# Optimization experiments

Hardware: AMD Instinct MI355X
Metric: run time of the kernel (lower is better)

The kernel has to match this reference:

```python
import jax, jax.numpy as jnp
import numpy as np

GROUPS = 8
EPS = 1e-3  # keras GroupNormalization default epsilon


def group_norm(x, gamma, beta):
    # x: [B,H,W,C], groups over channel axis
    B, H, W, C = x.shape
    g = GROUPS
    xr = x.reshape(B, H, W, g, C // g)
    mean = jnp.mean(xr, axis=(1, 2, 4), keepdims=True)
    var = jnp.var(xr, axis=(1, 2, 4), keepdims=True)
    xn = (xr - mean) * jax.lax.rsqrt(var + EPS)
    xn = xn.reshape(B, H, W, C)
    return xn * gamma + beta


def setup_inputs() -> dict:
    key = jax.random.key(0)
    ks = jax.random.split(key, 6)
    B, H, W, C = 8, 64, 64, 64
    std = 0.02
    return {
        "x": jax.random.normal(ks[0], (B, H, W, C), dtype=jnp.float32),
        "gamma": jnp.ones((C,), dtype=jnp.float32),
        "beta": jnp.zeros((C,), dtype=jnp.float32),
        "wq": jax.random.normal(ks[1], (C, C), dtype=jnp.float32) * std,
        "bq": jnp.zeros((C,), dtype=jnp.float32),
        "wk": jax.random.normal(ks[2], (C, C), dtype=jnp.float32) * std,
        "bk": jnp.zeros((C,), dtype=jnp.float32),
        "wv": jax.random.normal(ks[3], (C, C), dtype=jnp.float32) * std,
        "bv": jnp.zeros((C,), dtype=jnp.float32),
        "wp": jax.random.normal(ks[4], (C, C), dtype=jnp.float32) * std,
        "bp": jnp.zeros((C,), dtype=jnp.float32),
    }


def reference(x, gamma, beta, wq, bq, wk, bk, wv, bv, wp, bp):
    B, H, W, C = x.shape
    scale = jnp.asarray(C, x.dtype) ** -0.5
    h = group_norm(x, gamma, beta)  # note: residual uses normalized input (as in source)
    q = h @ wq + bq
    k = h @ wk + bk
    v = h @ wv + bv
    # full O((HW)^2) score tensor, exactly as the original
    attn = jnp.einsum('bhwc,bHWc->bhwHW', q, k) * scale
    attn = jax.nn.softmax(attn.reshape(B, H, W, H * W), axis=-1)
    attn = attn.reshape(B, H, W, H, W)
    proj = jnp.einsum('bhwHW,bHWc->bhwc', attn, v)
    proj = proj @ wp + bp
    return h + proj
```

## Files before the change

kernel.cpp:

```cpp
#include <hip/hip_runtime.h>

#define NTOK 4096
#define CH 64
#define LOG2E 1.4426950408889634f
#define QK_SCALE 0.42466090014400953f

typedef __bf16 bf8 __attribute__((ext_vector_type(8)));
typedef __bf16 bf4 __attribute__((ext_vector_type(4)));
typedef _Float16 h8 __attribute__((ext_vector_type(8)));
typedef _Float16 h4 __attribute__((ext_vector_type(4)));
typedef float f4 __attribute__((ext_vector_type(4)));
typedef long lx2 __attribute__((ext_vector_type(2)));

__device__ __forceinline__ f4 mfma16(bf8 a, bf8 b, f4 c) {
    return __builtin_amdgcn_mfma_f32_16x16x32_bf16(a, b, c, 0, 0, 0);
}
__device__ __forceinline__ f4 mfma8(long a, long b, f4 c) {
    return __builtin_amdgcn_mfma_f32_16x16x32_fp8_fp8(a, b, c, 0, 0, 0);
}
__device__ __forceinline__ unsigned char to_fp8(float v) {
    return (unsigned char)(__builtin_amdgcn_cvt_pk_fp8_f32(v, v, 0, false) & 0xff);
}

__global__ __launch_bounds__(256) void pre_kernel(const float* __restrict__ wq,
                                                  const float* __restrict__ wk,
                                                  const float* __restrict__ wv,
                                                  const float* __restrict__ wp,
                                                  const float* __restrict__ x,
                                                  __bf16* __restrict__ wqt,
                                                  __bf16* __restrict__ wkt,
                                                  __bf16* __restrict__ wvt,
                                                  __bf16* __restrict__ wpt,
                                                  float* __restrict__ gpart) {
    int t = threadIdx.x;
    if (blockIdx.x < 4) {
        int m = blockIdx.x;
        const float* src = (m == 0) ? wq : (m == 1) ? wk : (m == 2) ? wv : wp;
        __bf16* dst      = (m == 0) ? wqt : (m == 1) ? wkt : (m == 2) ? wvt : wpt;
        __shared__ float s[64][65];
        for (int i = 0; i < 16; ++i) {
            int e = i * 256 + t;
            s[e >> 6][e & 63] = src[e];
        }
        __syncthreads();
        int o = t >> 2, seg = t & 3;
        for (int j = 0; j < 16; ++j) {
            int in = seg * 16 + j;
            dst[o * 64 + in] = (__bf16)s[in][o];
        }
        return;
    }
    int bid = blockIdx.x - 4;
    int b = bid >> 6, slab = bid & 63;
    const float4* xb = (const float4*)(x + (size_t)(b * NTOK + slab * 64) * CH);
    float s = 0.f, ss = 0.f;
    for (int i = 0; i < 4; ++i) {
        int row = (t >> 4) + i * 16;
        float4 v = xb[row * 16 + (t & 15)];
        s  += v.x + v.y + v.z + v.w;
        ss += v.x * v.x + v.y * v.y + v.z * v.z + v.w * v.w;
    }
    __shared__ float ls[256], lss[256];
    ls[t] = s; lss[t] = ss;
    __syncthreads();
    if (t < 8) {
        float a = 0.f, aa = 0.f;
        for (int p = 0; p < 16; ++p) {
            a  += ls[p * 16 + 2 * t]  + ls[p * 16 + 2 * t + 1];
            aa += lss[p * 16 + 2 * t] + lss[p * 16 + 2 * t + 1];
        }
        gpart[((b * 64 + slab) * 8 + t) * 2 + 0] = a;
        gpart[((b * 64 + slab) * 8 + t) * 2 + 1] = aa;
    }
}

__global__ __launch_bounds__(256) void qkv_gn(const float* __restrict__ x,
                                              const float* __restrict__ gpart,
                                              const float* __restrict__ gamma,
                                              const float* __restrict__ beta,
                                              const __bf16* __restrict__ wqt,
                                              const __bf16* __restrict__ wkt,
                                              const __bf16* __restrict__ wvt,
                                              const float* __restrict__ bq,
                                              const float* __restrict__ bk,
                                              const float* __restrict__ bv,
                                              unsigned char* __restrict__ qp,
                                              unsigned char* __restrict__ kp,
                                              unsigned char* __restrict__ vp) {
    __shared__ __bf16 W[3][64][72];
    __shared__ _Float16 Vst[64][68];
    __shared__ unsigned char Qst[64][72];
    __shared__ unsigned char Kst[64][72];
    __shared__ float red[128];
    __shared__ float sstat[16];
    __shared__ float sg[64], sb2[64];
    int t = threadIdx.x;
    size_t rowbase = (size_t)blockIdx.x * 64;
    int b = (int)(rowbase >> 12), tokbase = (int)(rowbase & 4095);
    int lane = t & 63, wave = t >> 6, quad = lane >> 4, l15 = lane & 15;
    int row = wave * 16 + l15;

    const float* xr = x + (rowbase + row) * 64;
    float4 xl0 = *(const float4*)(xr + quad * 8);
    float4 xl1 = *(const float4*)(xr + quad * 8 + 4);
    float4 xh0 = *(const float4*)(xr + 32 + quad * 8);
    float4 xh1 = *(const float4*)(xr + 32 + quad * 8 + 4);

    for (int m = 0; m < 3; ++m) {
        const __bf16* src = (m == 0) ? wqt : (m == 1) ? wkt : wvt;
        for (int i = 0; i < 2; ++i) {
            int e = i * 256 + t, rr = e >> 3, ch = e & 7;
            *(bf8*)&W[m][rr][ch * 8] = *(const bf8*)(src + rr * 64 + ch * 8);
        }
    }
    if (t < 64) { sg[t] = gamma[t]; sb2[t] = beta[t]; }
    if (t < 64) {
        int gi = t & 7, c = t >> 3;
        const float2* gp = (const float2*)gpart + (size_t)b * 512 + gi;
        float a = 0.f, aa = 0.f;
        for (int p = c * 8; p < c * 8 + 8; ++p) {
            float2 v = gp[(size_t)p * 8];
            a += v.x; aa += v.y;
        }
        red[t * 2] = a; red[t * 2 + 1] = aa;
    }
    __syncthreads();
    if (t < 8) {
        float a = 0.f, aa = 0.f;
        for (int c = 0; c < 8; ++c) {
            a  += red[(c * 8 + t) * 2];
            aa += red[(c * 8 + t) * 2 + 1];
        }
        float mean = a * (1.f / 32768.f);
        float var = aa * (1.f / 32768.f) - mean * mean;
        sstat[t * 2 + 0] = mean;
        sstat[t * 2 + 1] = rsqrtf(var + 1e-3f);
    }
    __syncthreads();

    bf8 a0, a1;
    {
        float mlo = sstat[quad * 2], rlo = sstat[quad * 2 + 1];
        float mhi = sstat[(4 + quad) * 2], rhi = sstat[(4 + quad) * 2 + 1];
        float xl[8] = {xl0.x, xl0.y, xl0.z, xl0.w, xl1.x, xl1.y, xl1.z, xl1.w};
        float xh[8] = {xh0.x, xh0.y, xh0.z, xh0.w, xh1.x, xh1.y, xh1.z, xh1.w};
#pragma unroll
        for (int j = 0; j < 8; ++j) {
            int c = quad * 8 + j;
            a0[j] = (__bf16)((xl[j] - mlo) * sg[c] * rlo + sb2[c]);
            a1[j] = (__bf16)((xh[j] - mhi) * sg[32 + c] * rhi + sb2[32 + c]);
        }
    }

    for (int m = 0; m < 3; ++m) {
        const float* bias = (m == 0) ? bq : (m == 1) ? bk : bv;
        float sc = (m == 2) ? 1.0f : QK_SCALE;
        for (int tt = 0; tt < 4; ++tt) {
            int col = l15 + 16 * tt;
            bf8 b0 = *(const bf8*)&W[m][col][quad * 8];
            bf8 b1 = *(const bf8*)&W[m][col][32 + quad * 8];
            f4 acc = {0.f, 0.f, 0.f, 0.f};
            acc = mfma16(a0, b0, acc);
            acc = mfma16(a1, b1, acc);
            float bb = bias[col];
            if (m == 2) {
                for (int r = 0; r < 4; ++r)
                    Vst[col][wave * 16 + quad * 4 + r] = (_Float16)(acc[r] + bb);
            } else if (m == 1) {
                for (int r = 0; r < 4; ++r)
                    Kst[wave * 16 + quad * 4 + r][col] = to_fp8((acc[r] + bb) * sc);
            } else {
                for (int r = 0; r < 4; ++r)
                    Qst[wave * 16 + quad * 4 + r][col] = to_fp8((acc[r] + bb) * sc);
            }
        }
    }
    __syncthreads();
    {
        const unsigned char* krow = &Kst[wave * 16 + l15][0];
        lx2 kk; kk[0] = *(const long*)(krow + quad * 8);
        kk[1] = *(const long*)(krow + 32 + quad * 8);
        *(lx2*)(kp + (((size_t)b * 256 + (tokbase >> 4) + wave) * 64 + lane) * 16) = kk;
        const unsigned char* qrow = &Qst[wave * 16 + l15][0];
        lx2 qq; qq[0] = *(const long*)(qrow + quad * 8);
        qq[1] = *(const long*)(qrow + 32 + quad * 8);
        *(lx2*)(qp + (((size_t)b * 256 + (tokbase >> 4) + wave) * 64 + lane) * 16) = qq;
    }
    {
        int d = wave * 16 + l15;
        for (int kb = 0; kb < 2; ++kb) {
            h4 lo = *(const h4*)&Vst[d][kb * 32 + quad * 4];
            h4 hi = *(const h4*)&Vst[d][kb * 32 + 16 + quad * 4];
            int d0 = __builtin_amdgcn_cvt_pk_fp8_f32((float)lo[0], (float)lo[1], 0, false);
            d0     = __builtin_amdgcn_cvt_pk_fp8_f32((float)lo[2], (float)lo[3], d0, true);
            int d1 = __builtin_amdgcn_cvt_pk_fp8_f32((float)hi[0], (float)hi[1], 0, false);
            d1     = __builtin_amdgcn_cvt_pk_fp8_f32((float)hi[2], (float)hi[3], d1, true);
            long v8 = (long)(unsigned int)d0 | ((long)d1 << 32);
            int kt = (tokbase >> 5) + kb;
            *(long*)(vp + ((((size_t)b * 128 + kt) * 2 + (wave >> 1)) * 64 + lane) * 16
                        + (wave & 1) * 8) = v8;
        }
    }
}

__device__ __forceinline__ void load_kv(const unsigned char* kpw, const unsigned char* vpw,
                                        long kf[4], long vf[4]) {
    lx2 a = *(const lx2*)(kpw);
    lx2 b = *(const lx2*)(kpw + 1024);
    lx2 c = *(const lx2*)(vpw);
    lx2 d = *(const lx2*)(vpw + 1024);
    kf[0] = a[0]; kf[1] = a[1]; kf[2] = b[0]; kf[3] = b[1];
    vf[0] = c[0]; vf[1] = c[1]; vf[2] = d[0]; vf[3] = d[1];
}

__device__ __forceinline__ void compute32(const long kf[4], const long vf[4],
                                          const long aqlo[8], const long aqhi[8],
                                          long ones, f4 acc[8][4], f4 acc_li[8]) {
#pragma unroll
    for (int s = 0; s < 8; ++s) {
        f4 St0 = {0.f, 0.f, 0.f, 0.f};
        f4 St1 = {0.f, 0.f, 0.f, 0.f};
        St0 = mfma8(kf[0], aqlo[s], St0);
        St0 = mfma8(kf[1], aqhi[s], St0);
        St1 = mfma8(kf[2], aqlo[s], St1);
        St1 = mfma8(kf[3], aqhi[s], St1);
        float p00 = __builtin_amdgcn_exp2f(St0[0]);
        float p01 = __builtin_amdgcn_exp2f(St0[1]);
        float p02 = __builtin_amdgcn_exp2f(St0[2]);
        float p03 = __builtin_amdgcn_exp2f(St0[3]);
        float p10 = __builtin_amdgcn_exp2f(St1[0]);
        float p11 = __builtin_amdgcn_exp2f(St1[1]);
        float p12 = __builtin_amdgcn_exp2f(St1[2]);
        float p13 = __builtin_amdgcn_exp2f(St1[3]);
        int d0 = __builtin_amdgcn_cvt_pk_fp8_f32(p00, p01, 0, false);
        d0     = __builtin_amdgcn_cvt_pk_fp8_f32(p02, p03, d0, true);
        int d1 = __builtin_amdgcn_cvt_pk_fp8_f32(p10, p11, 0, false);
        d1     = __builtin_amdgcn_cvt_pk_fp8_f32(p12, p13, d1, true);
        long pf = (long)(unsigned int)d0 | ((long)d1 << 32);
        acc_li[s] = mfma8(ones, pf, acc_li[s]);
        acc[s][0] = mfma8(vf[0], pf, acc[s][0]);
        acc[s][1] = mfma8(vf[1], pf, acc[s][1]);
        acc[s][2] = mfma8(vf[2], pf, acc[s][2]);
        acc[s][3] = mfma8(vf[3], pf, acc[s][3]);
    }
}

__global__ __launch_bounds__(256, 1) void attn_final(const unsigned char* __restrict__ qp,
                                                     const unsigned char* __restrict__ kp,
                                                     const unsigned char* __restrict__ vp,
                                                     const __bf16* __restrict__ wpt,
                                                     const float* __restrict__ bp,
                                                     const float* __restrict__ x,
                                                     const float* __restrict__ gpart,
                                                     const float* __restrict__ gamma,
                                                     const float* __restrict__ beta,
                                                     float* __restrict__ out) {
    __shared__ _Float16 Om[2][128][72];
    __shared__ float sS[2][128];
    __shared__ __bf16 Wl[64][72];
    __shared__ __bf16 Ol[128][72];
    __shared__ float red[128];
    __shared__ float sstat[16], sg[64], sb[64];

    int bid = blockIdx.x;
    int qt = bid >> 3, b = bid & 7;
    int t = threadIdx.x, lane = t & 63, w = t >> 6, quad = lane >> 4, l15 = lane & 15;

    for (int i = 0; i < 2; ++i) {
        int e = i * 256 + t, row = e >> 3, ch = e & 7;
        *(bf8*)&Wl[row][ch * 8] = *(const bf8*)(wpt + row * 64 + ch * 8);
    }
    if (t < 64) { sg[t] = gamma[t]; sb[t] = beta[t]; }
    if (t < 64) {
        int gi = t & 7, c = t >> 3;
        const float2* gp = (const float2*)gpart + (size_t)b * 512 + gi;
        float a = 0.f, aa = 0.f;
        for (int p = c * 8; p < c * 8 + 8; ++p) {
            float2 v = gp[(size_t)p * 8];
            a += v.x; aa += v.y;
        }
        red[t * 2] = a; red[t * 2 + 1] = aa;
    }

    const unsigned char* qpb = qp + (((size_t)b * 256 + qt * 8) * 64 + lane) * 16;
    long aqlo[8], aqhi[8];
#pragma unroll
    for (int s = 0; s < 8; ++s) {
        lx2 qq = *(const lx2*)(qpb + (size_t)s * 1024);
        aqlo[s] = qq[0]; aqhi[s] = qq[1];
    }
    const unsigned char* kpw = kp + ((size_t)b * 256 + w * 64) * 1024 + lane * 16;
    const unsigned char* vpw = vp + ((size_t)b * 128 + w * 32) * 2048 + lane * 16;

    const long ones = 0x3838383838383838L;

    f4 acc[8][4] = {};
    f4 acc_li[8] = {};

    long kfA[4], kfB[4], vfA[4], vfB[4];
    load_kv(kpw, vpw, kfA, vfA);
    for (int it = 0; it < 32; it += 2) {
        load_kv(kpw + (size_t)(it + 1) * 2048, vpw + (size_t)(it + 1) * 2048, kfB, vfB);
        __builtin_amdgcn_s_setprio(1);
        compute32(kfA, vfA, aqlo, aqhi, ones, acc, acc_li);
        __builtin_amdgcn_s_setprio(0);
        if (it + 2 < 32)
            load_kv(kpw + (size_t)(it + 2) * 2048, vpw + (size_t)(it + 2) * 2048, kfA, vfA);
        __builtin_amdgcn_s_setprio(1);
        compute32(kfB, vfB, aqlo, aqhi, ones, acc, acc_li);
        __builtin_amdgcn_s_setprio(0);
    }

    float li[8];
#pragma unroll
    for (int s = 0; s < 8; ++s) li[s] = acc_li[s][0];

    if (w >= 2) {
        for (int s = 0; s < 8; ++s) {
            for (int td = 0; td < 4; ++td) {
                h4 o4;
                for (int r = 0; r < 4; ++r) o4[r] = (_Float16)acc[s][td][r];
                *(h4*)&Om[w - 2][s * 16 + l15][td * 16 + quad * 4] = o4;
            }
            if (quad == 0) sS[w - 2][s * 16 + l15] = li[s];
        }
    }
    __syncthreads();
    if (t < 8) {
        float a = 0.f, aa = 0.f;
        for (int c = 0; c < 8; ++c) {
            a  += red[(c * 8 + t) * 2];
            aa += red[(c * 8 + t) * 2 + 1];
        }
        float mean = a * (1.f / 32768.f);
        float var = aa * (1.f / 32768.f) - mean * mean;
        sstat[t * 2 + 0] = mean;
        sstat[t * 2 + 1] = rsqrtf(var + 1e-3f);
    }
    if (w < 2) {
        for (int s = 0; s < 8; ++s) {
            for (int td = 0; td < 4; ++td) {
                h4 o4 = *(const h4*)&Om[w][s * 16 + l15][td * 16 + quad * 4];
                for (int r = 0; r < 4; ++r) acc[s][td][r] += (float)o4[r];
            }
            li[s] += sS[w][s * 16 + l15];
        }
    }
    __syncthreads();
    if (w < 2) {
        for (int s = 0; s < 8; ++s) {
            for (int td = 0; td < 4; ++td) {
                h4 o4;
                for (int r = 0; r < 4; ++r) o4[r] = (_Float16)acc[s][td][r];
                *(h4*)&Om[w][s * 16 + l15][td * 16 + quad * 4] = o4;
            }
            if (quad == 0) sS[w][s * 16 + l15] = li[s];
        }
    }
    __syncthreads();
    {
        for (int half = 0; half < 2; ++half) {
            int idx = half * 256 + t;
            int qq = idx >> 2, ds = (idx & 3) * 16;
            float inv = 1.f / (sS[0][qq] + sS[1][qq]);
            h8 a0 = *(const h8*)&Om[0][qq][ds];
            h8 b0 = *(const h8*)&Om[0][qq][ds + 8];
            h8 a1 = *(const h8*)&Om[1][qq][ds];
            h8 b1 = *(const h8*)&Om[1][qq][ds + 8];
            bf8 olo, ohi;
            for (int j = 0; j < 8; ++j) {
                olo[j] = (__bf16)(((float)a0[j] + (float)a1[j]) * inv);
                ohi[j] = (__bf16)(((float)b0[j] + (float)b1[j]) * inv);
            }
            *(bf8*)&Ol[qq][ds] = olo;
            *(bf8*)&Ol[qq][ds + 8] = ohi;
        }
    }
    __syncthreads();
    for (int sr = 0; sr < 2; ++sr) {
        int r16 = w * 32 + sr * 16;
        size_t rowbase = ((size_t)b * NTOK + qt * 128) + r16;
        bf8 a0 = *(const bf8*)&Ol[r16 + l15][quad * 8];
        bf8 a1 = *(const bf8*)&Ol[r16 + l15][32 + quad * 8];
        for (int tt = 0; tt < 4; ++tt) {
            int col = l15 + 16 * tt;
            bf8 b0 = *(const bf8*)&Wl[col][quad * 8];
            bf8 b1 = *(const bf8*)&Wl[col][32 + quad * 8];
            f4 pacc = {0.f, 0.f, 0.f, 0.f};
            pacc = mfma16(a0, b0, pacc);
            pacc = mfma16(a1, b1, pacc);
            int grp = col >> 3;
            float mean = sstat[grp * 2], gs = sg[col] * sstat[grp * 2 + 1], bs = sb[col];
            float bias = bp[col];
            for (int r = 0; r < 4; ++r) {
                size_t gi = (rowbase + quad * 4 + r) * 64 + col;
                float h = (x[gi] - mean) * gs + bs;
                out[gi] = pacc[r] + bias + h;
            }
        }
    }
}

extern "C" void kernel_launch(void* const* d_in, const int* in_sizes, int n_in,
                              void* d_out, int out_size, void* d_ws, size_t ws_size,
                              hipStream_t stream) {
    const float* x     = (const float*)d_in[0];
    const float* gamma = (const float*)d_in[1];
    const float* beta  = (const float*)d_in[2];
    const float* wq    = (const float*)d_in[3];
    const float* bq    = (const float*)d_in[4];
    const float* wk    = (const float*)d_in[5];
    const float* bk    = (const float*)d_in[6];
    const float* wv    = (const float*)d_in[7];
    const float* bv    = (const float*)d_in[8];
    const float* wp    = (const float*)d_in[9];
    const float* bp    = (const float*)d_in[10];
    float* out = (float*)d_out;

    char* ws = (char*)d_ws;
    const size_t MB = 1024 * 1024;
    unsigned char* qpb = (unsigned char*)(ws);
    unsigned char* kpb = (unsigned char*)(ws + 2 * MB);
    unsigned char* vpb = (unsigned char*)(ws + 4 * MB);
    __bf16*   wqt  = (__bf16*)(ws + 12 * MB);
    __bf16*   wkt  = (__bf16*)(ws + 12 * MB + 8192);
    __bf16*   wvt  = (__bf16*)(ws + 12 * MB + 16384);
    __bf16*   wpt  = (__bf16*)(ws + 12 * MB + 24576);
    float*    gpart = (float*)(ws + 12 * MB + 32768);

    pre_kernel<<<516, 256, 0, stream>>>(wq, wk, wv, wp, x, wqt, wkt, wvt, wpt, gpart);
    qkv_gn<<<512, 256, 0, stream>>>(x, gpart, gamma, beta, wqt, wkt, wvt, bq, bk, bv,
                                    qpb, kpb, vpb);
    attn_final<<<256, 256, 0, stream>>>(qpb, kpb, vpb, wpt, bp, x, gpart, gamma, beta, out);
}
```

Baseline: 137.0 us.

## Split attention KV range across eight waves with two-level LDS reduction

The attention kernel now launches 512 threads per block instead of 256. Each of the eight waves processes half as many key/value tiles, and the partial accumulators are combined through a two-stage shared-memory tree reduction (waves 4-7 into 0-3, then 2-3 into 0-1). This raises the number of waves per CU, since the grid has only 256 blocks, so more latency can be hidden in the KV loop. The cost is extra reduction passes, barriers and roughly double the LDS for the partial-output buffers.

Result: faster. 120.0 us (-12.4%).

```diff
diff --git a/kernel.cpp b/kernel.cpp
--- a/kernel.cpp
+++ b/kernel.cpp
@@ -245,7 +245,7 @@
     }
 }
 
-__global__ __launch_bounds__(256, 1) void attn_final(const unsigned char* __restrict__ qp,
+__global__ __launch_bounds__(512, 1) void attn_final(const unsigned char* __restrict__ qp,
                                                      const unsigned char* __restrict__ kp,
                                                      const unsigned char* __restrict__ vp,
                                                      const __bf16* __restrict__ wpt,
@@ -255,8 +255,8 @@
                                                      const float* __restrict__ gamma,
                                                      const float* __restrict__ beta,
                                                      float* __restrict__ out) {
-    __shared__ _Float16 Om[2][128][72];
-    __shared__ float sS[2][128];
+    __shared__ _Float16 Om[4][128][72];
+    __shared__ float sS[4][128];
     __shared__ __bf16 Wl[64][72];
     __shared__ __bf16 Ol[128][72];
     __shared__ float red[128];
@@ -266,11 +266,11 @@
     int qt = bid >> 3, b = bid & 7;
     int t = threadIdx.x, lane = t & 63, w = t >> 6, quad = lane >> 4, l15 = lane & 15;
 
-    for (int i = 0; i < 2; ++i) {
-        int e = i * 256 + t, row = e >> 3, ch = e & 7;
+    {
+        int row = t >> 3, ch = t & 7;
         *(bf8*)&Wl[row][ch * 8] = *(const bf8*)(wpt + row * 64 + ch * 8);
     }
-    if (t < 64) { sg[t] = gamma[t]; sb[t] = beta[t]; }
+    if (t >= 64 && t < 128) { int u = t - 64; sg[u] = gamma[u]; sb[u] = beta[u]; }
     if (t < 64) {
         int gi = t & 7, c = t >> 3;
         const float2* gp = (const float2*)gpart + (size_t)b * 512 + gi;
@@ -289,8 +289,8 @@
         lx2 qq = *(const lx2*)(qpb + (size_t)s * 1024);
         aqlo[s] = qq[0]; aqhi[s] = qq[1];
     }
-    const unsigned char* kpw = kp + ((size_t)b * 256 + w * 64) * 1024 + lane * 16;
-    const unsigned char* vpw = vp + ((size_t)b * 128 + w * 32) * 2048 + lane * 16;
+    const unsigned char* kpw = kp + ((size_t)b * 256 + w * 32) * 1024 + lane * 16;
+    const unsigned char* vpw = vp + ((size_t)b * 128 + w * 16) * 2048 + lane * 16;
 
     const long ones = 0x3838383838383838L;
 
@@ -299,12 +299,12 @@
 
     long kfA[4], kfB[4], vfA[4], vfB[4];
     load_kv(kpw, vpw, kfA, vfA);
-    for (int it = 0; it < 32; it += 2) {
+    for (int it = 0; it < 16; it += 2) {
         load_kv(kpw + (size_t)(it + 1) * 2048, vpw + (size_t)(it + 1) * 2048, kfB, vfB);
         __builtin_amdgcn_s_setprio(1);
         compute32(kfA, vfA, aqlo, aqhi, ones, acc, acc_li);
         __builtin_amdgcn_s_setprio(0);
-        if (it + 2 < 32)
+        if (it + 2 < 16)
             load_kv(kpw + (size_t)(it + 2) * 2048, vpw + (size_t)(it + 2) * 2048, kfA, vfA);
         __builtin_amdgcn_s_setprio(1);
         compute32(kfB, vfB, aqlo, aqhi, ones, acc, acc_li);
@@ -315,7 +315,39 @@
 #pragma unroll
     for (int s = 0; s < 8; ++s) li[s] = acc_li[s][0];
 
-    if (w >= 2) {
+    if (w >= 4) {
+        for (int s = 0; s < 8; ++s) {
+            for (int td = 0; td < 4; ++td) {
+                h4 o4;
+                for (int r = 0; r < 4; ++r) o4[r] = (_Float16)acc[s][td][r];
+                *(h4*)&Om[w - 4][s * 16 + l15][td * 16 + quad * 4] = o4;
+            }
+            if (quad == 0) sS[w - 4][s * 16 + l15] = li[s];
+        }
+    }
+    __syncthreads();
+    if (t < 8) {
+        float a = 0.f, aa = 0.f;
+        for (int c = 0; c < 8; ++c) {
+            a  += red[(c * 8 + t) * 2];
+            aa += red[(c * 8 + t) * 2 + 1];
+        }
+        float mean = a * (1.f / 32768.f);
+        float var = aa * (1.f / 32768.f) - mean * mean;
+        sstat[t * 2 + 0] = mean;
+        sstat[t * 2 + 1] = rsqrtf(var + 1e-3f);
+    }
+    if (w < 4) {
+        for (int s = 0; s < 8; ++s) {
+            for (int td = 0; td < 4; ++td) {
+                h4 o4 = *(const h4*)&Om[w][s * 16 + l15][td * 16 + quad * 4];
+                for (int r = 0; r < 4; ++r) acc[s][td][r] += (float)o4[r];
+            }
+            li[s] += sS[w][s * 16 + l15];
+        }
+    }
+    __syncthreads();
+    if (w >= 2 && w < 4) {
         for (int s = 0; s < 8; ++s) {
             for (int td = 0; td < 4; ++td) {
                 h4 o4;
@@ -326,17 +358,6 @@
         }
     }
     __syncthreads();
-    if (t < 8) {
-        float a = 0.f, aa = 0.f;
-        for (int c = 0; c < 8; ++c) {
-            a  += red[(c * 8 + t) * 2];
-            aa += red[(c * 8 + t) * 2 + 1];
-        }
-        float mean = a * (1.f / 32768.f);
-        float var = aa * (1.f / 32768.f) - mean * mean;
-        sstat[t * 2 + 0] = mean;
-        sstat[t * 2 + 1] = rsqrtf(var + 1e-3f);
-    }
     if (w < 2) {
         for (int s = 0; s < 8; ++s) {
             for (int td = 0; td < 4; ++td) {
@@ -359,29 +380,25 @@
     }
     __syncthreads();
     {
-        for (int half = 0; half < 2; ++half) {
-            int idx = half * 256 + t;
-            int qq = idx >> 2, ds = (idx & 3) * 16;
-            float inv = 1.f / (sS[0][qq] + sS[1][qq]);
-            h8 a0 = *(const h8*)&Om[0][qq][ds];
-            h8 b0 = *(const h8*)&Om[0][qq][ds + 8];
-            h8 a1 = *(const h8*)&Om[1][qq][ds];
-            h8 b1 = *(const h8*)&Om[1][qq][ds + 8];
-            bf8 olo, ohi;
-            for (int j = 0; j < 8; ++j) {
-                olo[j] = (__bf16)(((float)a0[j] + (float)a1[j]) * inv);
-                ohi[j] = (__bf16)(((float)b0[j] + (float)b1[j]) * inv);
-            }
-            *(bf8*)&Ol[qq][ds] = olo;
-            *(bf8*)&Ol[qq][ds + 8] = ohi;
-        }
-    }
-    __syncthreads();
-    for (int sr = 0; sr < 2; ++sr) {
-        int r16 = w * 32 + sr * 16;
-        size_t rowbase = ((size_t)b * NTOK + qt * 128) + r16;
-        bf8 a0 = *(const bf8*)&Ol[r16 + l15][quad * 8];
-        bf8 a1 = *(const bf8*)&Ol[r16 + l15][32 + quad * 8];
+        int qq = t >> 2, ds = (t & 3) * 16;
+        float inv = 1.f / (sS[0][qq] + sS[1][qq]);
+        h8 a0 = *(const h8*)&Om[0][qq][ds];
+        h8 b0 = *(const h8*)&Om[0][qq][ds + 8];
+        h8 a1 = *(const h8*)&Om[1][qq][ds];
+        h8 b1 = *(const h8*)&Om[1][qq][ds + 8];
+        bf8 olo, ohi;
+        for (int j = 0; j < 8; ++j) {
+            olo[j] = (__bf16)(((float)a0[j] + (float)a1[j]) * inv);
+            ohi[j] = (__bf16)(((float)b0[j] + (float)b1[j]) * inv);
+        }
+        *(bf8*)&Ol[qq][ds] = olo;
+        *(bf8*)&Ol[qq][ds + 8] = ohi;
+    }
+    __syncthreads();
+    {
+        size_t rowbase = ((size_t)b * NTOK + qt * 128) + w * 16;
+        bf8 a0 = *(const bf8*)&Ol[w * 16 + l15][quad * 8];
+        bf8 a1 = *(const bf8*)&Ol[w * 16 + l15][32 + quad * 8];
         for (int tt = 0; tt < 4; ++tt) {
             int col = l15 + 16 * tt;
             bf8 b0 = *(const bf8*)&Wl[col][quad * 8];
@@ -431,5 +448,5 @@
     pre_kernel<<<516, 256, 0, stream>>>(wq, wk, wv, wp, x, wqt, wkt, wvt, wpt, gpart);
     qkv_gn<<<512, 256, 0, stream>>>(x, gpart, gamma, beta, wqt, wkt, wvt, bq, bk, bv,
                                     qpb, kpb, vpb);
-    attn_final<<<256, 256, 0, stream>>>(qpb, kpb, vpb, wpt, bp, x, gpart, gamma, beta, out);
-}
+    attn_final<<<256, 512, 0, stream>>>(qpb, kpb, vpb, wpt, bp, x, gpart, gamma, beta, out);
+}
```
